# Kernel optimization log

Hardware: AMD Instinct MI355X
Metric: run time of the kernel (lower is better)

Reference implementation:

```python
import jax, jax.numpy as jnp
import numpy as np

N_NODES = 2048
N_EDGES = 32768
N_GRAPH = 64
D_INJ = 240
D_EMB = 480
D_FEAT = 512
H = 4
DH = 120
SH_DIM = 9
N_RBF = 128
CUTOFF = 5.0
AVG_DEGREE = 16.0
AVG_NUM_NODES = 32.0
N_ITER = 2
MAX_ATOM = 64


def _ln(x):
    mu = jnp.mean(x, axis=-1, keepdims=True)
    var = jnp.var(x, axis=-1, keepdims=True)
    return (x - mu) * jax.lax.rsqrt(var + 1e-6)


def _sph(u):
    # component-normalized real spherical harmonics l=0,1,2 of unit vectors u [E,3]
    x, y, z = u[:, 0], u[:, 1], u[:, 2]
    s3 = np.sqrt(3.0); s15 = np.sqrt(15.0); s5 = np.sqrt(5.0)
    return jnp.stack([
        jnp.ones_like(x),
        s3 * x, s3 * y, s3 * z,
        s15 * x * y, s15 * y * z,
        0.5 * s5 * (3.0 * z * z - 1.0),
        s15 * x * z, 0.5 * s15 * (x * x - y * y)], axis=-1)


def _block(z, esrc, edst, sh, rbf, Wq, Wk, Wv, Wsh, Wr, Wo, F1, F2, res_ffn):
    # equivariant-style dot-product attention: gather -> edge compute -> segment softmax -> scatter
    x = _ln(z)
    q = (x @ Wq)[edst].reshape(-1, H, DH)
    k = (x @ Wk)[esrc].reshape(-1, H, DH)
    v = (x @ Wv)[esrc].reshape(-1, H, DH)
    m = (sh @ Wsh).reshape(-1, H, DH)          # SH tensor-product message modulation
    r = jax.nn.silu(rbf @ Wr)[:, :, None]      # radial gate per head [E,H,1]
    k = (k + m) * r
    v = (v + m) * r
    logit = jnp.sum(q * k, axis=-1) / np.sqrt(DH)   # [E,H]
    mx = jax.ops.segment_max(logit, edst, num_segments=N_NODES)
    mx = jnp.where(jnp.isfinite(mx), mx, 0.0)
    ex = jnp.exp(logit - mx[edst])
    den = jax.ops.segment_sum(ex, edst, num_segments=N_NODES)
    alpha = ex / (den[edst] + 1e-9)
    agg = jax.ops.segment_sum(alpha[:, :, None] * v, edst, num_segments=N_NODES)
    y = z + agg.reshape(N_NODES, H * DH) @ Wo
    out = jax.nn.silu(_ln(y) @ F1) @ F2
    return y + out if res_ffn else out


def _forward(pos, atom_table, degWr, degWsh,
             b0_Wq, b0_Wk, b0_Wv, b0_Wsh, b0_Wr, b0_Wo, b0_F1, b0_F2,
             bm_Wq, bm_Wk, bm_Wv, bm_Wsh, bm_Wr, bm_Wo, bm_F1, bm_F2,
             bf_Wq, bf_Wk, bf_Wv, bf_Wsh, bf_Wr, bf_Wo, bf_F1, bf_F2,
             hW1, hW2, node_atom, edge_src, edge_dst, batch):
    # ---- encode ----
    vec = pos[edge_src] - pos[edge_dst]
    d = jnp.sqrt(jnp.sum(vec * vec, axis=-1) + 1e-12)
    sh = _sph(vec / d[:, None])                              # [E,9]
    centers = jnp.linspace(0.0, CUTOFF, N_RBF)
    width = CUTOFF / N_RBF
    rbf = jnp.exp(-0.5 * jnp.square((d[:, None] - centers) / width))  # [E,128]
    atom = atom_table[node_atom]                             # [N,240]
    rad = jax.nn.silu(rbf @ degWr)                           # [E,9]
    deg = jax.ops.segment_sum((sh * rad) @ degWsh, edge_dst, num_segments=N_NODES) / AVG_DEGREE
    inj = atom + deg                                         # input-injection features
    # ---- DEQ fixed-point (unrolled) ----
    z = jnp.zeros((N_NODES, D_EMB), dtype=pos.dtype)
    for _ in range(N_ITER):
        z = _block(jnp.concatenate([z, inj], axis=-1), edge_src, edge_dst, sh, rbf,
                   b0_Wq, b0_Wk, b0_Wv, b0_Wsh, b0_Wr, b0_Wo, b0_F1, b0_F2, False)
        for i in range(4):
            z = _block(z, edge_src, edge_dst, sh, rbf,
                       bm_Wq[i], bm_Wk[i], bm_Wv[i], bm_Wsh[i], bm_Wr[i],
                       bm_Wo[i], bm_F1[i], bm_F2[i], True)
    # ---- decode ----
    feat = _block(z, edge_src, edge_dst, sh, rbf,
                  bf_Wq, bf_Wk, bf_Wv, bf_Wsh, bf_Wr, bf_Wo, bf_F1, bf_F2, False)
    feat = _ln(feat)
    e_node = jax.nn.silu(feat @ hW1) @ hW2                   # [N,1]
    return jax.ops.segment_sum(e_node, batch, num_segments=N_GRAPH) / np.sqrt(AVG_NUM_NODES)


def setup_inputs() -> dict:
    key = jax.random.key(0)
    it = iter(jax.random.split(key, 40))
    def nrm(shape):
        fan = shape[-2] if len(shape) >= 2 else shape[-1]
        return jax.random.normal(next(it), shape, jnp.float32) / np.sqrt(fan)
    inp = {}
    inp['pos'] = jax.random.normal(next(it), (N_NODES, 3), jnp.float32) * 2.0
    inp['node_atom'] = jax.random.randint(next(it), (N_NODES,), 0, MAX_ATOM)
    inp['edge_src'] = jax.random.randint(next(it), (N_EDGES,), 0, N_NODES)
    inp['edge_dst'] = jax.random.randint(next(it), (N_EDGES,), 0, N_NODES)
    inp['batch'] = jnp.sort(jax.random.randint(next(it), (N_NODES,), 0, N_GRAPH))
    inp['atom_table'] = nrm((MAX_ATOM, D_INJ))
    inp['degWr'] = nrm((N_RBF, SH_DIM))
    inp['degWsh'] = nrm((SH_DIM, D_INJ))
    DZ = D_EMB + D_INJ
    inp['b0_Wq'] = nrm((DZ, H * DH)); inp['b0_Wk'] = nrm((DZ, H * DH)); inp['b0_Wv'] = nrm((DZ, H * DH))
    inp['b0_Wsh'] = nrm((SH_DIM, H * DH)); inp['b0_Wr'] = nrm((N_RBF, H))
    inp['b0_Wo'] = nrm((H * DH, DZ)); inp['b0_F1'] = nrm((DZ, D_EMB)); inp['b0_F2'] = nrm((D_EMB, D_EMB))
    inp['bm_Wq'] = nrm((4, D_EMB, H * DH)); inp['bm_Wk'] = nrm((4, D_EMB, H * DH)); inp['bm_Wv'] = nrm((4, D_EMB, H * DH))
    inp['bm_Wsh'] = nrm((4, SH_DIM, H * DH)); inp['bm_Wr'] = nrm((4, N_RBF, H))
    inp['bm_Wo'] = nrm((4, H * DH, D_EMB)); inp['bm_F1'] = nrm((4, D_EMB, D_EMB)); inp['bm_F2'] = nrm((4, D_EMB, D_EMB))
    inp['bf_Wq'] = nrm((D_EMB, H * DH)); inp['bf_Wk'] = nrm((D_EMB, H * DH)); inp['bf_Wv'] = nrm((D_EMB, H * DH))
    inp['bf_Wsh'] = nrm((SH_DIM, H * DH)); inp['bf_Wr'] = nrm((N_RBF, H))
    inp['bf_Wo'] = nrm((H * DH, D_EMB)); inp['bf_F1'] = nrm((D_EMB, D_EMB)); inp['bf_F2'] = nrm((D_EMB, D_FEAT))
    inp['hW1'] = nrm((D_FEAT, D_FEAT)); inp['hW2'] = nrm((D_FEAT, 1))
    return inp


def reference(pos, atom_table, degWr, degWsh,
              b0_Wq, b0_Wk, b0_Wv, b0_Wsh, b0_Wr, b0_Wo, b0_F1, b0_F2,
              bm_Wq, bm_Wk, bm_Wv, bm_Wsh, bm_Wr, bm_Wo, bm_F1, bm_F2,
              bf_Wq, bf_Wk, bf_Wv, bf_Wsh, bf_Wr, bf_Wo, bf_F1, bf_F2,
              hW1, hW2, node_atom, edge_src, edge_dst, batch):
    return _forward(pos, atom_table, degWr, degWsh,
                    b0_Wq, b0_Wk, b0_Wv, b0_Wsh, b0_Wr, b0_Wo, b0_F1, b0_F2,
                    bm_Wq, bm_Wk, bm_Wv, bm_Wsh, bm_Wr, bm_Wo, bm_F1, bm_F2,
                    bf_Wq, bf_Wk, bf_Wv, bf_Wsh, bf_Wr, bf_Wo, bf_F1, bf_F2,
                    hW1, hW2, node_atom, edge_src, edge_dst, batch)
```

## Files before the change

### kernel.cpp

```cpp
#include <hip/hip_runtime.h>

#define NN 2048
#define NE 32768
#define NG 64
#define DINJ 240
#define DEMB 480
#define DFEAT 512
#define MAXDEG 192

typedef unsigned short ushort_t;
typedef __attribute__((ext_vector_type(8))) short short8;
typedef __attribute__((ext_vector_type(4))) float floatx4;

__device__ __forceinline__ float b2f(ushort_t u){
  union { unsigned u; float f; } x; x.u = ((unsigned)u) << 16; return x.f;
}
__device__ __forceinline__ ushort_t f2b(float f){
  union { float f; unsigned u; } x; x.f = f;
  unsigned r = x.u + 0x7FFFu + ((x.u >> 16) & 1u);
  return (ushort_t)(r >> 16);
}
__device__ __forceinline__ float wredsum(float v){
  #pragma unroll
  for (int o = 32; o > 0; o >>= 1) v += __shfl_xor(v, o, 64);
  return v;
}
__device__ __forceinline__ float silu_f(float x){ return x / (1.f + __expf(-x)); }

__global__ void zero_f32(float* p, int n){
  int i = blockIdx.x*256 + threadIdx.x; if (i < n) p[i] = 0.f;
}

__global__ void detect_kernel(const ushort_t* __restrict__ probe, int* flag){
  __shared__ int c;
  if (threadIdx.x == 0) c = 0;
  __syncthreads();
  ushort_t u = probe[2*threadIdx.x];
  int e = (u >> 7) & 0xFF;
  int plausible = (u == 0) || (e >= 100 && e <= 140);
  atomicAdd(&c, plausible);
  __syncthreads();
  if (threadIdx.x == 0) *flag = (c >= 192) ? 0 : 1;
}

struct CDesc { const void* src; float* dst; int n; };
struct CDescArr { CDesc d[11]; };
__global__ __launch_bounds__(256) void convert_inputs(CDescArr ca, const int* __restrict__ flag){
  CDesc cd = ca.d[blockIdx.y];
  int isf32 = *flag;
  for (int i = blockIdx.x*256 + threadIdx.x; i < cd.n; i += gridDim.x*256){
    cd.dst[i] = isf32 ? ((const float*)cd.src)[i] : b2f(((const ushort_t*)cd.src)[i]);
  }
}

struct TDesc { const void* src; ushort_t* dh; ushort_t* dl; int K; int M; int Kpad; int Mpad; int eoff; };
struct TDescArr { TDesc d[37]; };
__global__ __launch_bounds__(256) void transpose_all(TDescArr ta, const int* __restrict__ flag){
  TDesc td = ta.d[blockIdx.z];
  int k0 = blockIdx.x*32, m0 = blockIdx.y*32;
  if (k0 >= td.Kpad || m0 >= td.Mpad) return;
  int isf32 = *flag;
  __shared__ float lds[32*33];
  int tx = threadIdx.x & 31, ty = threadIdx.x >> 5;
  #pragma unroll
  for (int r = 0; r < 4; ++r){
    int kl = ty + r*8;
    int k = k0 + kl, mm = m0 + tx;
    float x = 0.f;
    if (k < td.K && mm < td.M){
      size_t si = (size_t)td.eoff + (size_t)k*td.M + mm;
      x = isf32 ? ((const float*)td.src)[si] : b2f(((const ushort_t*)td.src)[si]);
    }
    lds[kl*33 + tx] = x;
  }
  __syncthreads();
  #pragma unroll
  for (int r = 0; r < 4; ++r){
    int nl = ty + r*8;
    int n = m0 + nl, k = k0 + tx;
    if (n < td.Mpad && k < td.Kpad){
      float x = lds[tx*33 + nl];
      ushort_t h = f2b(x);
      size_t di = (size_t)n*td.Kpad + k;
      td.dh[di] = h;
      td.dl[di] = f2b(x - b2f(h));
    }
  }
}

__global__ void pack_wr(const float* __restrict__ b0Wr, const float* __restrict__ bmWr,
                        const float* __restrict__ bfWr, float* __restrict__ Wr_all){
  int idx = blockIdx.x*256 + threadIdx.x; if (idx >= 128*24) return;
  int k = idx / 24, o = idx - k*24;
  int slot = o >> 2, h = o & 3;
  const float* Wr = (slot == 0) ? b0Wr : ((slot <= 4) ? bmWr + (size_t)(slot-1)*512 : bfWr);
  Wr_all[idx] = Wr[k*4+h];
}

__global__ __launch_bounds__(128) void edge_all_kernel(
    const float* __restrict__ pos,
    const int* __restrict__ esrc, const int* __restrict__ edst,
    const float* __restrict__ degWr, const float* __restrict__ Wr_all,
    float* __restrict__ sh_out, float* __restrict__ t9,
    float* __restrict__ r_all){
  __shared__ float w9L[128*9];
  __shared__ float w24L[128*24];
  int t = threadIdx.x;
  for (int i = t; i < 128*9; i += 128)  w9L[i]  = degWr[i];
  for (int i = t; i < 128*24; i += 128) w24L[i] = Wr_all[i];
  __syncthreads();
  int e = blockIdx.x*128 + t; if (e >= NE) return;
  int s = esrc[e], d = edst[e];
  float x = pos[s*3+0] - pos[d*3+0];
  float y = pos[s*3+1] - pos[d*3+1];
  float z = pos[s*3+2] - pos[d*3+2];
  float dd = sqrtf(x*x + y*y + z*z + 1e-12f);
  float ix = x/dd, iy = y/dd, iz = z/dd;
  const float s3 = 1.7320508075688772f, s15 = 3.872983346207417f, s5 = 2.23606797749979f;
  float sh[9];
  sh[0] = 1.f; sh[1] = s3*ix; sh[2] = s3*iy; sh[3] = s3*iz;
  sh[4] = s15*ix*iy; sh[5] = s15*iy*iz; sh[6] = 0.5f*s5*(3.f*iz*iz - 1.f);
  sh[7] = s15*ix*iz; sh[8] = 0.5f*s15*(ix*ix - iy*iy);
  #pragma unroll
  for (int j = 0; j < 9; ++j) sh_out[(size_t)e*9+j] = sh[j];
  float t9a[9], ga[24];
  #pragma unroll
  for (int j = 0; j < 9; ++j) t9a[j] = 0.f;
  #pragma unroll
  for (int o = 0; o < 24; ++o) ga[o] = 0.f;
  for (int k = 0; k < 128; ++k){
    float c = (float)k * (5.0f/127.0f);
    float u = (dd - c) * (128.0f/5.0f);
    float rb = __expf(-0.5f*u*u);
    const float* w9  = w9L + k*9;
    const float* w24 = w24L + k*24;
    #pragma unroll
    for (int j = 0; j < 9; ++j) t9a[j] += rb*w9[j];
    #pragma unroll
    for (int o = 0; o < 24; ++o) ga[o] += rb*w24[o];
  }
  #pragma unroll
  for (int j = 0; j < 9; ++j) t9[(size_t)e*9+j] = sh[j]*silu_f(t9a[j]);
  #pragma unroll
  for (int o = 0; o < 24; ++o){
    int slot = o >> 2, h = o & 3;
    r_all[((size_t)slot*NE + e)*4 + h] = silu_f(ga[o]);
  }
}

__global__ void hist_kernel(const int* __restrict__ edst, int* counts){
  int e = blockIdx.x*256 + threadIdx.x; if (e < NE) atomicAdd(&counts[edst[e]], 1);
}
__global__ __launch_bounds__(1024) void scan_kernel(const int* __restrict__ counts,
                                                    int* rowptr, int* cursor){
  __shared__ int s[1024];
  int t = threadIdx.x;
  int c0 = counts[2*t], c1 = counts[2*t+1];
  s[t] = c0 + c1;
  __syncthreads();
  for (int off = 1; off < 1024; off <<= 1){
    int v = (t >= off) ? s[t-off] : 0;
    __syncthreads();
    s[t] += v;
    __syncthreads();
  }
  int excl = s[t] - (c0 + c1);
  rowptr[2*t]   = excl;       cursor[2*t]   = excl;
  rowptr[2*t+1] = excl + c0;  cursor[2*t+1] = excl + c0;
  if (t == 1023) rowptr[2048] = s[1023];
}
__global__ void scatter_kernel(const int* __restrict__ edst, int* cursor, int* perm){
  int e = blockIdx.x*256 + threadIdx.x; if (e >= NE) return;
  int p = atomicAdd(&cursor[edst[e]], 1);
  perm[p] = e;
}

__global__ __launch_bounds__(64) void inj_kernel(const float* __restrict__ t9,
    const int* __restrict__ rowptr, const int* __restrict__ perm,
    const int* __restrict__ node_atom, const float* __restrict__ atom_table,
    const float* __restrict__ degWsh, float* __restrict__ inj){
  int i = blockIdx.x; int lane = threadIdx.x;
  int b = rowptr[i], e = rowptr[i+1];
  float T[9];
  #pragma unroll
  for (int j = 0; j < 9; ++j) T[j] = 0.f;
  for (int idx = b; idx < e; ++idx){
    int ed = perm[idx];
    #pragma unroll
    for (int j = 0; j < 9; ++j) T[j] += t9[(size_t)ed*9+j];
  }
  int a = node_atom[i];
  for (int c = lane; c < DINJ; c += 64){
    float s = 0.f;
    #pragma unroll
    for (int j = 0; j < 9; ++j) s += T[j]*degWsh[j*DINJ+c];
    inj[(size_t)i*DINJ+c] = atom_table[(size_t)a*DINJ+c] + s*(1.0f/16.0f);
  }
}

__global__ __launch_bounds__(256) void ln_kernel(const float* __restrict__ in, int D,
                                                 int Kpad, ushort_t* __restrict__ oh){
  int i = blockIdx.x*4 + (threadIdx.x >> 6);
  int lane = threadIdx.x & 63;
  const float* row = in + (size_t)i*D;
  float s = 0.f, sq = 0.f;
  for (int d = lane; d < D; d += 64){ float x = row[d]; s += x; sq += x*x; }
  s = wredsum(s); sq = wredsum(sq);
  float mu = s / (float)D;
  float var = fmaxf(sq / (float)D - mu*mu, 0.f);
  float rs = rsqrtf(var + 1e-6f);
  ushort_t* ohrow = oh + (size_t)i*Kpad;
  for (int d = lane; d < D; d += 64) ohrow[d] = f2b((row[d]-mu)*rs);
  for (int d = D + lane; d < Kpad; d += 64) ohrow[d] = 0;
}

__global__ __launch_bounds__(256) void ln_cat_kernel(const float* __restrict__ z,
    const float* __restrict__ inj, ushort_t* __restrict__ oh){
  int i = blockIdx.x*4 + (threadIdx.x >> 6);
  int lane = threadIdx.x & 63;
  const float* zr = z + (size_t)i*480;
  const float* ir = inj + (size_t)i*240;
  float s = 0.f, sq = 0.f;
  for (int d = lane; d < 720; d += 64){
    float x = (d < 480) ? zr[d] : ir[d-480];
    s += x; sq += x*x;
  }
  s = wredsum(s); sq = wredsum(sq);
  float mu = s * (1.0f/720.0f);
  float var = fmaxf(sq * (1.0f/720.0f) - mu*mu, 0.f);
  float rs = rsqrtf(var + 1e-6f);
  ushort_t* ohrow = oh + (size_t)i*736;
  for (int d = lane; d < 720; d += 64){
    float x = (d < 480) ? zr[d] : ir[d-480];
    ohrow[d] = f2b((x-mu)*rs);
  }
  for (int d = 720 + lane; d < 736; d += 64) ohrow[d] = 0;
}

template<int KPAD, bool SPLITB>
__global__ __launch_bounds__(256) void gemm_bt(
    const ushort_t* __restrict__ A,
    const ushort_t* __restrict__ BTh, const ushort_t* __restrict__ BTl,
    int N, int ldc,
    float* __restrict__ Cf, ushort_t* __restrict__ Cb,
    const float* __restrict__ R, const float* __restrict__ R2, int flags){
  int lane = threadIdx.x & 63, wave = threadIdx.x >> 6;
  int row0 = blockIdx.y*64 + (wave>>1)*32;
  int col0 = blockIdx.x*64 + (wave&1)*32;
  int m = lane & 15, q4 = lane >> 4;
  size_t a0 = (size_t)(row0+m)*KPAD + q4*8;
  size_t a1 = a0 + (size_t)16*KPAD;
  size_t b0 = (size_t)(col0+m)*KPAD + q4*8;
  size_t b1 = b0 + (size_t)16*KPAD;
  floatx4 acc00 = {0,0,0,0}, acc01 = {0,0,0,0}, acc10 = {0,0,0,0}, acc11 = {0,0,0,0};
  constexpr int steps = KPAD >> 5;
  constexpr int DEPTH = SPLITB ? 3 : 4;
  struct Frag { short8 A0, A1, B0h, B1h, B0l, B1l; };
  auto loadF = [&](int s) -> Frag {
    Frag f;
    size_t o = (size_t)s*32;
    f.A0  = *(const short8*)(A   + a0 + o);
    f.A1  = *(const short8*)(A   + a1 + o);
    f.B0h = *(const short8*)(BTh + b0 + o);
    f.B1h = *(const short8*)(BTh + b1 + o);
    if (SPLITB){
      f.B0l = *(const short8*)(BTl + b0 + o);
      f.B1l = *(const short8*)(BTl + b1 + o);
    }
    return f;
  };
  Frag ring[DEPTH];
  #pragma unroll
  for (int d = 0; d < DEPTH; ++d) ring[d] = loadF(d < steps ? d : steps-1);
  #pragma unroll
  for (int s = 0; s < steps; ++s){
    Frag cur = ring[s % DEPTH];
    if (s + DEPTH < steps) ring[s % DEPTH] = loadF(s + DEPTH);
    acc00 = __builtin_amdgcn_mfma_f32_16x16x32_bf16(cur.A0, cur.B0h, acc00, 0, 0, 0);
    acc01 = __builtin_amdgcn_mfma_f32_16x16x32_bf16(cur.A0, cur.B1h, acc01, 0, 0, 0);
    acc10 = __builtin_amdgcn_mfma_f32_16x16x32_bf16(cur.A1, cur.B0h, acc10, 0, 0, 0);
    acc11 = __builtin_amdgcn_mfma_f32_16x16x32_bf16(cur.A1, cur.B1h, acc11, 0, 0, 0);
    if (SPLITB){
      acc00 = __builtin_amdgcn_mfma_f32_16x16x32_bf16(cur.A0, cur.B0l, acc00, 0, 0, 0);
      acc01 = __builtin_amdgcn_mfma_f32_16x16x32_bf16(cur.A0, cur.B1l, acc01, 0, 0, 0);
      acc10 = __builtin_amdgcn_mfma_f32_16x16x32_bf16(cur.A1, cur.B0l, acc10, 0, 0, 0);
      acc11 = __builtin_amdgcn_mfma_f32_16x16x32_bf16(cur.A1, cur.B1l, acc11, 0, 0, 0);
    }
  }
  #pragma unroll
  for (int rr = 0; rr < 2; ++rr){
    #pragma unroll
    for (int cc = 0; cc < 2; ++cc){
      int col = col0 + cc*16 + m;
      if (col >= N) continue;
      floatx4 acc = rr ? (cc ? acc11 : acc10) : (cc ? acc01 : acc00);
      int rowb = row0 + rr*16 + q4*4;
      #pragma unroll
      for (int r = 0; r < 4; ++r){
        int row = rowb + r;
        size_t idx = (size_t)row*ldc + col;
        float v = acc[r];
        if (flags & 2){
          if (flags & 8)
            v += (col < 480) ? R[(size_t)row*480 + col] : R2[(size_t)row*240 + (col-480)];
          else
            v += R[idx];
        }
        if (flags & 1) v = silu_f(v);
        if (flags & 4) Cb[idx] = f2b(v);
        else           Cf[idx] = v;
      }
    }
  }
}

__global__ __launch_bounds__(256) void node_attn_kernel(
    const float* __restrict__ qkv, const float* __restrict__ sh,
    const float* __restrict__ Wsh, const float* __restrict__ r_slot,
    const int* __restrict__ rowptr, const int* __restrict__ perm,
    const int* __restrict__ esrc, ushort_t* __restrict__ aggh){
  int i = blockIdx.x; int t = threadIdx.x;
  int lane = t & 63, w = t >> 6;
  int b = rowptr[i]; int deg = min(rowptr[i+1] - b, MAXDEG);
  __shared__ float qL[480];
  __shared__ float PqL[36];
  __shared__ float logitL[MAXDEG*4];
  __shared__ float rL[MAXDEG*4];
  __shared__ int eL[MAXDEG], srcL[MAXDEG];
  __shared__ float S[36];
  __shared__ float mxs[4], dens[4];
  for (int d = t; d < 480; d += 256) qL[d] = qkv[(size_t)i*1440 + d];
  for (int idx = t; idx < deg; idx += 256){
    int e = perm[b+idx];
    eL[idx] = e;
    srcL[idx] = esrc[e];
  }
  __syncthreads();
  if (t < 36){
    int h = t/9, j = t - h*9;
    const float* ws = Wsh + (size_t)j*DEMB + h*120;
    const float* qh = qL + h*120;
    float p = 0.f;
    for (int k = 0; k < 120; ++k) p += qh[k]*ws[k];
    PqL[t] = p;
  }
  __syncthreads();
  const float inv = 0.091287092917527686f;
  for (int base = 0; base < deg; base += 64){
    int idx = base + (t >> 2);
    if (idx < deg){
      int h = t & 3;
      int e = eL[idx], s = srcL[idx];
      const float4* kk = (const float4*)(qkv + (size_t)s*1440 + 480 + h*120);
      const float4* qq = (const float4*)(qL + h*120);
      float p = 0.f;
      #pragma unroll
      for (int it = 0; it < 30; ++it){
        float4 a = qq[it], bb = kk[it];
        p += a.x*bb.x + a.y*bb.y + a.z*bb.z + a.w*bb.w;
      }
      float mmq = 0.f;
      const float* she = sh + (size_t)e*9;
      #pragma unroll
      for (int j = 0; j < 9; ++j) mmq += she[j]*PqL[h*9+j];
      float rr = r_slot[(size_t)e*4+h];
      rL[idx*4+h] = rr;
      logitL[idx*4+h] = rr*(p + mmq)*inv;
    }
  }
  __syncthreads();
  float mx = -1e30f;
  for (int idx = lane; idx < deg; idx += 64) mx = fmaxf(mx, logitL[idx*4+w]);
  #pragma unroll
  for (int o = 32; o > 0; o >>= 1) mx = fmaxf(mx, __shfl_xor(mx, o, 64));
  if (deg == 0) mx = 0.f;
  float den = 0.f;
  for (int idx = lane; idx < deg; idx += 64) den += __expf(logitL[idx*4+w]-mx);
  den = wredsum(den) + 1e-9f;
  if (lane == 0){ mxs[w] = mx; dens[w] = den; }
  __syncthreads();
  for (int j = t; j < deg*4; j += 256){
    int h = j & 3;
    logitL[j] = __expf(logitL[j]-mxs[h]) / dens[h] * rL[j];
  }
  __syncthreads();
  float a0 = 0.f, a1 = 0.f;
  int d0 = 2*t, h2 = d0/120;
  if (t >= 240){
    for (int o = t - 240; o < 36; o += 16){
      int h = o/9, j = o - h*9;
      float a = 0.f;
      for (int idx = 0; idx < deg; ++idx)
        a += logitL[idx*4+h]*sh[(size_t)eL[idx]*9+j];
      S[o] = a;
    }
  } else {
    for (int idx = 0; idx < deg; ++idx){
      float wgt = logitL[idx*4+h2];
      float2 vv = *(const float2*)(qkv + (size_t)srcL[idx]*1440 + 960 + d0);
      a0 += wgt*vv.x; a1 += wgt*vv.y;
    }
  }
  __syncthreads();
  if (t < 240){
    float mm0 = 0.f, mm1 = 0.f;
    #pragma unroll
    for (int j = 0; j < 9; ++j){
      mm0 += S[h2*9+j]*Wsh[j*DEMB + d0];
      mm1 += S[h2*9+j]*Wsh[j*DEMB + d0 + 1];
    }
    aggh[(size_t)i*DEMB + d0]     = f2b(a0 + mm0);
    aggh[(size_t)i*DEMB + d0 + 1] = f2b(a1 + mm1);
  }
}

__global__ __launch_bounds__(256) void head_dot_kernel(const ushort_t* __restrict__ g1h,
    const float* __restrict__ hW2, const int* __restrict__ batch, float* gsum){
  int i = blockIdx.x*4 + (threadIdx.x >> 6);
  int lane = threadIdx.x & 63;
  float s = 0.f;
  for (int d = lane; d < DFEAT; d += 64)
    s += b2f(g1h[(size_t)i*DFEAT + d]) * hW2[d];
  s = wredsum(s);
  if (lane == 0) atomicAdd(&gsum[batch[i]], s);
}
__global__ void finalize_kernel(const float* __restrict__ gsum,
                                const int* __restrict__ flag, void* out){
  int g = threadIdx.x;
  if (g < NG){
    float v = gsum[g] * 0.17677669529663687f;
    if (*flag) ((float*)out)[g] = v;
    else       ((ushort_t*)out)[g] = f2b(v);
  }
}

extern "C" void kernel_launch(void* const* d_in, const int* in_sizes, int n_in,
                              void* d_out, int out_size, void* d_ws, size_t ws_size,
                              hipStream_t stream) {
  (void)in_sizes; (void)n_in; (void)out_size; (void)ws_size;
  const void* pos        = d_in[0];
  const int*  node_atom  = (const int*)d_in[1];
  const int*  esrc       = (const int*)d_in[2];
  const int*  edst       = (const int*)d_in[3];
  const int*  batch      = (const int*)d_in[4];
  const void* atom_table = d_in[5];
  const void* degWr      = d_in[6];
  const void* degWsh     = d_in[7];
  const void* b0_Wq  = d_in[8];
  const void* b0_Wk  = d_in[9];
  const void* b0_Wv  = d_in[10];
  const void* b0_Wsh = d_in[11];
  const void* b0_Wr  = d_in[12];
  const void* b0_Wo  = d_in[13];
  const void* b0_F1  = d_in[14];
  const void* b0_F2  = d_in[15];
  const void* bm_Wq  = d_in[16];
  const void* bm_Wk  = d_in[17];
  const void* bm_Wv  = d_in[18];
  const void* bm_Wsh = d_in[19];
  const void* bm_Wr  = d_in[20];
  const void* bm_Wo  = d_in[21];
  const void* bm_F1  = d_in[22];
  const void* bm_F2  = d_in[23];
  const void* bf_Wq  = d_in[24];
  const void* bf_Wk  = d_in[25];
  const void* bf_Wv  = d_in[26];
  const void* bf_Wsh = d_in[27];
  const void* bf_Wr  = d_in[28];
  const void* bf_Wo  = d_in[29];
  const void* bf_F1  = d_in[30];
  const void* bf_F2  = d_in[31];
  const void* hW1    = d_in[32];
  const void* hW2    = d_in[33];

  char* bws = (char*)d_ws;
  size_t off = 0;
  auto alloc = [&](size_t bytes) -> void* {
    void* p = bws + off;
    off += (bytes + 255) & ~(size_t)255;
    return p;
  };
  int* dflag   = (int*)alloc(256);
  float* sh_f  = (float*)alloc((size_t)NE*9*4);
  float* t9    = (float*)alloc((size_t)NE*9*4);
  int* counts  = (int*)alloc(2048*4);
  int* rowptr  = (int*)alloc(2049*4);
  int* cursor  = (int*)alloc(2048*4);
  int* perm    = (int*)alloc((size_t)NE*4);
  float* injb  = (float*)alloc((size_t)NN*DINJ*4);
  float* zA    = (float*)alloc((size_t)NN*512*4);
  float* zB    = (float*)alloc((size_t)NN*512*4);
  ushort_t* xlnh = (ushort_t*)alloc((size_t)NN*736*2);
  float* qkvb  = (float*)alloc((size_t)NN*1440*4);
  float* Wr_all = (float*)alloc((size_t)128*24*4);
  float* r_all = (float*)alloc((size_t)6*NE*4*4);
  ushort_t* aggh = (ushort_t*)alloc((size_t)NN*DEMB*2);
  float* ybuf  = (float*)alloc((size_t)NN*720*4);
  ushort_t* h1h = (ushort_t*)alloc((size_t)NN*DEMB*2);
  ushort_t* g1h = (ushort_t*)alloc((size_t)NN*DFEAT*2);
  float* gsum  = (float*)alloc(64*4);

  float* pos_c    = (float*)alloc((size_t)NN*3*4);
  float* atom_c   = (float*)alloc((size_t)64*DINJ*4);
  float* degWr_c  = (float*)alloc((size_t)128*9*4);
  float* degWsh_c = (float*)alloc((size_t)9*DINJ*4);
  float* b0_Wsh_c = (float*)alloc((size_t)9*480*4);
  float* b0_Wr_c  = (float*)alloc((size_t)128*4*4);
  float* bm_Wsh_c = (float*)alloc((size_t)4*9*480*4);
  float* bm_Wr_c  = (float*)alloc((size_t)4*128*4*4);
  float* bf_Wsh_c = (float*)alloc((size_t)9*480*4);
  float* bf_Wr_c  = (float*)alloc((size_t)128*4*4);
  float* hW2_c    = (float*)alloc((size_t)512*4);

  auto allocW = [&](size_t elems, ushort_t*& h, ushort_t*& l){
    h = (ushort_t*)alloc(elems*2); l = (ushort_t*)alloc(elems*2);
  };
  ushort_t *b0_qkvTh,*b0_qkvTl,*b0_WoTh,*b0_WoTl,*b0_F1Th,*b0_F1Tl,*b0_F2Th,*b0_F2Tl;
  allocW((size_t)1472*736, b0_qkvTh, b0_qkvTl);
  allocW((size_t)768*480,  b0_WoTh,  b0_WoTl);
  allocW((size_t)512*736,  b0_F1Th,  b0_F1Tl);
  allocW((size_t)512*480,  b0_F2Th,  b0_F2Tl);
  ushort_t *bm_qkvTh[4],*bm_qkvTl[4],*bm_WoTh[4],*bm_WoTl[4],*bm_F1Th[4],*bm_F1Tl[4],*bm_F2Th[4],*bm_F2Tl[4];
  for (int i = 0; i < 4; ++i){
    allocW((size_t)1472*480, bm_qkvTh[i], bm_qkvTl[i]);
    allocW((size_t)512*480,  bm_WoTh[i],  bm_WoTl[i]);
    allocW((size_t)512*480,  bm_F1Th[i],  bm_F1Tl[i]);
    allocW((size_t)512*480,  bm_F2Th[i],  bm_F2Tl[i]);
  }
  ushort_t *bf_qkvTh,*bf_qkvTl,*bf_WoTh,*bf_WoTl,*bf_F1Th,*bf_F1Tl,*bf_F2Th,*bf_F2Tl,*hW1Th,*hW1Tl;
  allocW((size_t)1472*480, bf_qkvTh, bf_qkvTl);
  allocW((size_t)512*480,  bf_WoTh,  bf_WoTl);
  allocW((size_t)512*480,  bf_F1Th,  bf_F1Tl);
  allocW((size_t)512*480,  bf_F2Th,  bf_F2Tl);
  allocW((size_t)512*512,  hW1Th,    hW1Tl);

  detect_kernel<<<1, 256, 0, stream>>>((const ushort_t*)atom_table, dflag);

  CDescArr ca;
  int ci = 0;
  auto addC = [&](const void* s, float* d, int n){
    ca.d[ci].src = s; ca.d[ci].dst = d; ca.d[ci].n = n; ++ci;
  };
  addC(pos, pos_c, NN*3);
  addC(atom_table, atom_c, 64*DINJ);
  addC(degWr, degWr_c, 128*9);
  addC(degWsh, degWsh_c, 9*DINJ);
  addC(b0_Wsh, b0_Wsh_c, 9*480);
  addC(b0_Wr, b0_Wr_c, 128*4);
  addC(bm_Wsh, bm_Wsh_c, 4*9*480);
  addC(bm_Wr, bm_Wr_c, 4*128*4);
  addC(bf_Wsh, bf_Wsh_c, 9*480);
  addC(bf_Wr, bf_Wr_c, 128*4);
  addC(hW2, hW2_c, 512);
  convert_inputs<<<dim3(8, 11), 256, 0, stream>>>(ca, dflag);

  TDescArr ta;
  int ti = 0;
  auto addT = [&](const void* s, ushort_t* dh, ushort_t* dl, int K, int M,
                  int Kp, int Mp, int rowoff, int eo){
    ta.d[ti].src = s;
    ta.d[ti].dh = dh + (size_t)rowoff*Kp;
    ta.d[ti].dl = dl + (size_t)rowoff*Kp;
    ta.d[ti].K = K; ta.d[ti].M = M; ta.d[ti].Kpad = Kp; ta.d[ti].Mpad = Mp;
    ta.d[ti].eoff = eo; ++ti;
  };
  addT(b0_Wq, b0_qkvTh, b0_qkvTl, 720, 480, 736, 480, 0,   0);
  addT(b0_Wk, b0_qkvTh, b0_qkvTl, 720, 480, 736, 480, 480, 0);
  addT(b0_Wv, b0_qkvTh, b0_qkvTl, 720, 480, 736, 512, 960, 0);
  addT(b0_Wo, b0_WoTh,  b0_WoTl,  480, 720, 480, 768, 0,   0);
  addT(b0_F1, b0_F1Th,  b0_F1Tl,  720, 480, 736, 512, 0,   0);
  addT(b0_F2, b0_F2Th,  b0_F2Tl,  480, 480, 480, 512, 0,   0);
  for (int i = 0; i < 4; ++i){
    int eo = i*480*480;
    addT(bm_Wq, bm_qkvTh[i], bm_qkvTl[i], 480, 480, 480, 480, 0,   eo);
    addT(bm_Wk, bm_qkvTh[i], bm_qkvTl[i], 480, 480, 480, 480, 480, eo);
    addT(bm_Wv, bm_qkvTh[i], bm_qkvTl[i], 480, 480, 480, 512, 960, eo);
    addT(bm_Wo, bm_WoTh[i],  bm_WoTl[i],  480, 480, 480, 512, 0,   eo);
    addT(bm_F1, bm_F1Th[i],  bm_F1Tl[i],  480, 480, 480, 512, 0,   eo);
    addT(bm_F2, bm_F2Th[i],  bm_F2Tl[i],  480, 480, 480, 512, 0,   eo);
  }
  addT(bf_Wq, bf_qkvTh, bf_qkvTl, 480, 480, 480, 480, 0,   0);
  addT(bf_Wk, bf_qkvTh, bf_qkvTl, 480, 480, 480, 480, 480, 0);
  addT(bf_Wv, bf_qkvTh, bf_qkvTl, 480, 480, 480, 512, 960, 0);
  addT(bf_Wo, bf_WoTh,  bf_WoTl,  480, 480, 480, 512, 0,   0);
  addT(bf_F1, bf_F1Th,  bf_F1Tl,  480, 480, 480, 512, 0,   0);
  addT(bf_F2, bf_F2Th,  bf_F2Tl,  480, 512, 480, 512, 0,   0);
  addT(hW1,   hW1Th,    hW1Tl,    512, 512, 512, 512, 0,   0);
  transpose_all<<<dim3(23, 24, 37), 256, 0, stream>>>(ta, dflag);

  pack_wr<<<12, 256, 0, stream>>>(b0_Wr_c, bm_Wr_c, bf_Wr_c, Wr_all);
  edge_all_kernel<<<NE/128, 128, 0, stream>>>(pos_c, esrc, edst, degWr_c, Wr_all,
                                              sh_f, t9, r_all);

  zero_f32<<<(2048 + 255)/256, 256, 0, stream>>>((float*)counts, 2048);
  hist_kernel<<<NE/256, 256, 0, stream>>>(edst, counts);
  scan_kernel<<<1, 1024, 0, stream>>>(counts, rowptr, cursor);
  scatter_kernel<<<NE/256, 256, 0, stream>>>(edst, cursor, perm);

  inj_kernel<<<NN, 64, 0, stream>>>(t9, rowptr, perm, node_atom, atom_c, degWsh_c, injb);
  zero_f32<<<(NN*DEMB)/256, 256, 0, stream>>>(zA, NN*DEMB);

  auto gemm = [&](const ushort_t* A, const ushort_t* BTh, const ushort_t* BTl,
                  int N, int Npad, int Kp, int ldc,
                  float* Cf, ushort_t* Cb, const float* R, const float* R2,
                  int flags, bool split){
    dim3 g(Npad/64, 32);
    if (split){
      if (Kp == 480)
        gemm_bt<480,true><<<g, 256, 0, stream>>>(A, BTh, BTl, N, ldc, Cf, Cb, R, R2, flags);
      else if (Kp == 512)
        gemm_bt<512,true><<<g, 256, 0, stream>>>(A, BTh, BTl, N, ldc, Cf, Cb, R, R2, flags);
      else
        gemm_bt<736,true><<<g, 256, 0, stream>>>(A, BTh, BTl, N, ldc, Cf, Cb, R, R2, flags);
    } else {
      if (Kp == 480)
        gemm_bt<480,false><<<g, 256, 0, stream>>>(A, BTh, BTl, N, ldc, Cf, Cb, R, R2, flags);
      else if (Kp == 512)
        gemm_bt<512,false><<<g, 256, 0, stream>>>(A, BTh, BTl, N, ldc, Cf, Cb, R, R2, flags);
      else
        gemm_bt<736,false><<<g, 256, 0, stream>>>(A, BTh, BTl, N, ldc, Cf, Cb, R, R2, flags);
    }
  };

  struct BW {
    const float *Wsh, *r_slot;
    const ushort_t *qkvTh,*qkvTl,*WoTh,*WoTl,*F1Th,*F1Tl,*F2Th,*F2Tl;
    int Din, Kpad, Dout; bool res;
  };
  auto run_block = [&](const BW& bw, const float* zin, const float* zinj, float* zout){
    if (zinj) ln_cat_kernel<<<NN/4, 256, 0, stream>>>(zin, zinj, xlnh);
    else      ln_kernel<<<NN/4, 256, 0, stream>>>(zin, bw.Din, bw.Kpad, xlnh);
    gemm(xlnh, bw.qkvTh, bw.qkvTl, 1440, 1472, bw.Kpad, 1440,
         qkvb, nullptr, nullptr, nullptr, 0, true);
    node_attn_kernel<<<NN, 256, 0, stream>>>(qkvb, sh_f, bw.Wsh, bw.r_slot,
                                             rowptr, perm, esrc, aggh);
    int WoNpad = (bw.Din == 720) ? 768 : 512;
    gemm(aggh, bw.WoTh, bw.WoTl, bw.Din, WoNpad, 480, bw.Din,
         ybuf, nullptr, zin, zinj, zinj ? (2|8) : 2, false);
    ln_kernel<<<NN/4, 256, 0, stream>>>(ybuf, bw.Din, bw.Kpad, xlnh);
    gemm(xlnh, bw.F1Th, bw.F1Tl, DEMB, 512, bw.Kpad, DEMB,
         nullptr, h1h, nullptr, nullptr, 1|4, false);
    gemm(h1h, bw.F2Th, bw.F2Tl, bw.Dout, 512, 480, bw.Dout,
         zout, nullptr, bw.res ? ybuf : nullptr, nullptr, bw.res ? 2 : 0, false);
  };

  BW b0 = { b0_Wsh_c, r_all + (size_t)0*NE*4,
            b0_qkvTh,b0_qkvTl,b0_WoTh,b0_WoTl,b0_F1Th,b0_F1Tl,b0_F2Th,b0_F2Tl,
            720, 736, 480, false };
  BW bm[4];
  for (int i = 0; i < 4; ++i){
    bm[i] = { bm_Wsh_c + (size_t)i*9*480, r_all + (size_t)(1+i)*NE*4,
              bm_qkvTh[i],bm_qkvTl[i],bm_WoTh[i],bm_WoTl[i],
              bm_F1Th[i],bm_F1Tl[i],bm_F2Th[i],bm_F2Tl[i],
              480, 480, 480, true };
  }
  BW bf = { bf_Wsh_c, r_all + (size_t)5*NE*4,
            bf_qkvTh,bf_qkvTl,bf_WoTh,bf_WoTl,bf_F1Th,bf_F1Tl,bf_F2Th,bf_F2Tl,
            480, 480, 512, false };

  float* z  = zA;
  float* z2 = zB;
  for (int iter = 0; iter < 2; ++iter){
    run_block(b0, z, injb, z2);
    { float* tmp = z; z = z2; z2 = tmp; }
    for (int i = 0; i < 4; ++i){
      run_block(bm[i], z, nullptr, z2);
      { float* tmp = z; z = z2; z2 = tmp; }
    }
  }
  run_block(bf, z, nullptr, z2);
  ln_kernel<<<NN/4, 256, 0, stream>>>(z2, DFEAT, DFEAT, xlnh);
  gemm(xlnh, hW1Th, hW1Tl, DFEAT, 512, DFEAT, DFEAT,
       nullptr, g1h, nullptr, nullptr, 1|4, true);
  zero_f32<<<1, 64, 0, stream>>>(gsum, 64);
  head_dot_kernel<<<NN/4, 256, 0, stream>>>(g1h, hW2_c, batch, gsum);
  finalize_kernel<<<1, 64, 0, stream>>>(gsum, dflag, d_out);
}
```

Before: 1.384 ms.

## Stage GEMM tiles through LDS with async global-to-LDS loads and double buffering

Replaces the register-ring GEMM, where each wave loaded its own fragments straight from global memory, with a shared-memory tiled GEMM. Tiles come in through global_load_lds direct copies into double-buffered LDS with an XOR swizzle, and are shared across the four waves. Each wave now computes a 16xRF by 64 tile, and the wide QKV GEMM uses 128-row blocks (RF=2). The aim is to cut redundant global loads of A and B and raise data reuse per block. In exchange it adds a barrier every K step, makes K a runtime value instead of a template constant, and launches fewer blocks for the wide GEMMs.

```diff
diff --git a/kernel.cpp b/kernel.cpp
--- a/kernel.cpp
+++ b/kernel.cpp
@@ -26,6 +26,12 @@
   return v;
 }
 __device__ __forceinline__ float silu_f(float x){ return x / (1.f + __expf(-x)); }
+
+__device__ __forceinline__ void gload16(const ushort_t* g, ushort_t* l){
+  __builtin_amdgcn_global_load_lds(
+      (const __attribute__((address_space(1))) unsigned int*)g,
+      (__attribute__((address_space(3))) unsigned int*)l, 16, 0, 0);
+}
 
 __global__ void zero_f32(float* p, int n){
   int i = blockIdx.x*256 + threadIdx.x; if (i < n) p[i] = 0.f;
@@ -237,69 +243,98 @@
   for (int d = 720 + lane; d < 736; d += 64) ohrow[d] = 0;
 }
 
-template<int KPAD, bool SPLITB>
-__global__ __launch_bounds__(256) void gemm_bt(
+template<int RF, bool SPLITB>
+__global__ __launch_bounds__(256) void gemm_lds(
     const ushort_t* __restrict__ A,
     const ushort_t* __restrict__ BTh, const ushort_t* __restrict__ BTl,
-    int N, int ldc,
+    int KPAD, int N, int ldc,
     float* __restrict__ Cf, ushort_t* __restrict__ Cb,
     const float* __restrict__ R, const float* __restrict__ R2, int flags){
-  int lane = threadIdx.x & 63, wave = threadIdx.x >> 6;
-  int row0 = blockIdx.y*64 + (wave>>1)*32;
-  int col0 = blockIdx.x*64 + (wave&1)*32;
+  constexpr int BM = 64*RF;
+  __shared__ alignas(16) ushort_t AsS[2*BM*32];
+  __shared__ alignas(16) ushort_t BsS[2*64*32];
+  __shared__ alignas(16) ushort_t BlS[SPLITB ? 2*64*32 : 16];
+  int lane = threadIdx.x & 63, w = threadIdx.x >> 6;
+  int row0 = blockIdx.y * BM;
+  int col0 = blockIdx.x * 64;
   int m = lane & 15, q4 = lane >> 4;
-  size_t a0 = (size_t)(row0+m)*KPAD + q4*8;
-  size_t a1 = a0 + (size_t)16*KPAD;
-  size_t b0 = (size_t)(col0+m)*KPAD + q4*8;
-  size_t b1 = b0 + (size_t)16*KPAD;
-  floatx4 acc00 = {0,0,0,0}, acc01 = {0,0,0,0}, acc10 = {0,0,0,0}, acc11 = {0,0,0,0};
-  constexpr int steps = KPAD >> 5;
-  constexpr int DEPTH = SPLITB ? 3 : 4;
-  struct Frag { short8 A0, A1, B0h, B1h, B0l, B1l; };
-  auto loadF = [&](int s) -> Frag {
-    Frag f;
-    size_t o = (size_t)s*32;
-    f.A0  = *(const short8*)(A   + a0 + o);
-    f.A1  = *(const short8*)(A   + a1 + o);
-    f.B0h = *(const short8*)(BTh + b0 + o);
-    f.B1h = *(const short8*)(BTh + b1 + o);
-    if (SPLITB){
-      f.B0l = *(const short8*)(BTl + b0 + o);
-      f.B1l = *(const short8*)(BTl + b1 + o);
-    }
-    return f;
+  int rsub = lane >> 2;
+  int sseg = (lane & 3) ^ (rsub & 3);
+  size_t gAo[RF];
+  #pragma unroll
+  for (int i = 0; i < RF; ++i)
+    gAo[i] = (size_t)(row0 + (w + i*4)*16 + rsub)*KPAD + sseg*8;
+  size_t gBo = (size_t)(col0 + w*16 + rsub)*KPAD + sseg*8;
+  int sw = (q4 ^ (m & 3))*8;
+  int Aoff[RF], Boff[4];
+  #pragma unroll
+  for (int i = 0; i < RF; ++i) Aoff[i] = (w*16*RF + i*16 + m)*32 + sw;
+  #pragma unroll
+  for (int j = 0; j < 4; ++j)  Boff[j] = (j*16 + m)*32 + sw;
+
+  auto stage = [&](int buf, int kblk){
+    int ko = kblk*32;
+    #pragma unroll
+    for (int i = 0; i < RF; ++i)
+      gload16(A + gAo[i] + ko, AsS + buf*BM*32 + (w + i*4)*512);
+    gload16(BTh + gBo + ko, BsS + buf*2048 + w*512);
+    if constexpr (SPLITB)
+      gload16(BTl + gBo + ko, BlS + buf*2048 + w*512);
   };
-  Frag ring[DEPTH];
-  #pragma unroll
-  for (int d = 0; d < DEPTH; ++d) ring[d] = loadF(d < steps ? d : steps-1);
-  #pragma unroll
+
+  floatx4 acc[RF][4];
+  #pragma unroll
+  for (int i = 0; i < RF; ++i)
+    #pragma unroll
+    for (int j = 0; j < 4; ++j) acc[i][j] = (floatx4){0,0,0,0};
+
+  int steps = KPAD >> 5;
+  stage(0, 0);
+  __syncthreads();
   for (int s = 0; s < steps; ++s){
-    Frag cur = ring[s % DEPTH];
-    if (s + DEPTH < steps) ring[s % DEPTH] = loadF(s + DEPTH);
-    acc00 = __builtin_amdgcn_mfma_f32_16x16x32_bf16(cur.A0, cur.B0h, acc00, 0, 0, 0);
-    acc01 = __builtin_amdgcn_mfma_f32_16x16x32_bf16(cur.A0, cur.B1h, acc01, 0, 0, 0);
-    acc10 = __builtin_amdgcn_mfma_f32_16x16x32_bf16(cur.A1, cur.B0h, acc10, 0, 0, 0);
-    acc11 = __builtin_amdgcn_mfma_f32_16x16x32_bf16(cur.A1, cur.B1h, acc11, 0, 0, 0);
-    if (SPLITB){
-      acc00 = __builtin_amdgcn_mfma_f32_16x16x32_bf16(cur.A0, cur.B0l, acc00, 0, 0, 0);
-      acc01 = __builtin_amdgcn_mfma_f32_16x16x32_bf16(cur.A0, cur.B1l, acc01, 0, 0, 0);
-      acc10 = __builtin_amdgcn_mfma_f32_16x16x32_bf16(cur.A1, cur.B0l, acc10, 0, 0, 0);
-      acc11 = __builtin_amdgcn_mfma_f32_16x16x32_bf16(cur.A1, cur.B1l, acc11, 0, 0, 0);
-    }
-  }
-  #pragma unroll
-  for (int rr = 0; rr < 2; ++rr){
-    #pragma unroll
-    for (int cc = 0; cc < 2; ++cc){
-      int col = col0 + cc*16 + m;
+    int cur = s & 1;
+    if (s + 1 < steps) stage(cur ^ 1, s + 1);
+    short8 a[RF], bh[4];
+    #pragma unroll
+    for (int i = 0; i < RF; ++i)
+      a[i] = *(const short8*)(AsS + cur*BM*32 + Aoff[i]);
+    #pragma unroll
+    for (int j = 0; j < 4; ++j)
+      bh[j] = *(const short8*)(BsS + cur*2048 + Boff[j]);
+    if constexpr (SPLITB){
+      short8 bl[4];
+      #pragma unroll
+      for (int j = 0; j < 4; ++j)
+        bl[j] = *(const short8*)(BlS + cur*2048 + Boff[j]);
+      #pragma unroll
+      for (int i = 0; i < RF; ++i)
+        #pragma unroll
+        for (int j = 0; j < 4; ++j){
+          acc[i][j] = __builtin_amdgcn_mfma_f32_16x16x32_bf16(a[i], bh[j], acc[i][j], 0, 0, 0);
+          acc[i][j] = __builtin_amdgcn_mfma_f32_16x16x32_bf16(a[i], bl[j], acc[i][j], 0, 0, 0);
+        }
+    } else {
+      #pragma unroll
+      for (int i = 0; i < RF; ++i)
+        #pragma unroll
+        for (int j = 0; j < 4; ++j)
+          acc[i][j] = __builtin_amdgcn_mfma_f32_16x16x32_bf16(a[i], bh[j], acc[i][j], 0, 0, 0);
+    }
+    __syncthreads();
+  }
+
+  #pragma unroll
+  for (int i = 0; i < RF; ++i){
+    int rowb = row0 + w*16*RF + i*16 + q4*4;
+    #pragma unroll
+    for (int j = 0; j < 4; ++j){
+      int col = col0 + j*16 + m;
       if (col >= N) continue;
-      floatx4 acc = rr ? (cc ? acc11 : acc10) : (cc ? acc01 : acc00);
-      int rowb = row0 + rr*16 + q4*4;
       #pragma unroll
       for (int r = 0; r < 4; ++r){
         int row = rowb + r;
         size_t idx = (size_t)row*ldc + col;
-        float v = acc[r];
+        float v = acc[i][j][r];
         if (flags & 2){
           if (flags & 8)
             v += (col < 480) ? R[(size_t)row*480 + col] : R2[(size_t)row*240 + (col-480)];
@@ -600,25 +635,22 @@
   inj_kernel<<<NN, 64, 0, stream>>>(t9, rowptr, perm, node_atom, atom_c, degWsh_c, injb);
   zero_f32<<<(NN*DEMB)/256, 256, 0, stream>>>(zA, NN*DEMB);
 
-  auto gemm = [&](const ushort_t* A, const ushort_t* BTh, const ushort_t* BTl,
+  auto gemm = [&](const ushort_t* Aop, const ushort_t* BTh, const ushort_t* BTl,
                   int N, int Npad, int Kp, int ldc,
                   float* Cf, ushort_t* Cb, const float* R, const float* R2,
                   int flags, bool split){
-    dim3 g(Npad/64, 32);
-    if (split){
-      if (Kp == 480)
-        gemm_bt<480,true><<<g, 256, 0, stream>>>(A, BTh, BTl, N, ldc, Cf, Cb, R, R2, flags);
-      else if (Kp == 512)
-        gemm_bt<512,true><<<g, 256, 0, stream>>>(A, BTh, BTl, N, ldc, Cf, Cb, R, R2, flags);
+    if (Npad >= 1024){
+      dim3 g(Npad/64, NN/128);
+      if (split)
+        gemm_lds<2,true><<<g, 256, 0, stream>>>(Aop, BTh, BTl, Kp, N, ldc, Cf, Cb, R, R2, flags);
       else
-        gemm_bt<736,true><<<g, 256, 0, stream>>>(A, BTh, BTl, N, ldc, Cf, Cb, R, R2, flags);
+        gemm_lds<2,false><<<g, 256, 0, stream>>>(Aop, BTh, BTl, Kp, N, ldc, Cf, Cb, R, R2, flags);
     } else {
-      if (Kp == 480)
-        gemm_bt<480,false><<<g, 256, 0, stream>>>(A, BTh, BTl, N, ldc, Cf, Cb, R, R2, flags);
-      else if (Kp == 512)
-        gemm_bt<512,false><<<g, 256, 0, stream>>>(A, BTh, BTl, N, ldc, Cf, Cb, R, R2, flags);
+      dim3 g(Npad/64, NN/64);
+      if (split)
+        gemm_lds<1,true><<<g, 256, 0, stream>>>(Aop, BTh, BTl, Kp, N, ldc, Cf, Cb, R, R2, flags);
       else
-        gemm_bt<736,false><<<g, 256, 0, stream>>>(A, BTh, BTl, N, ldc, Cf, Cb, R, R2, flags);
+        gemm_lds<1,false><<<g, 256, 0, stream>>>(Aop, BTh, BTl, Kp, N, ldc, Cf, Cb, R, R2, flags);
     }
   };
 
```

Measured after the change: 1.457 ms. 1.05x slower.
